# Optimization experiments

Hardware: AMD Instinct MI355X
Metric: run time of the kernel (lower is better)

The kernel has to match this reference:

```python
import jax, jax.numpy as jnp
import numpy as np
from jax import lax

B, S, D, E, H = 2, 2048, 1024, 8, 4096


def setup_inputs() -> dict:
    key = jax.random.key(0)
    ks = jax.random.split(key, 10)
    sc = 0.02  # GPT-style init scale
    return {
        "x": jax.random.normal(ks[0], (B, S, D), jnp.float32),
        "noise": jax.random.normal(ks[1], (B, S, E), jnp.float32),
        "w_route": jax.random.normal(ks[2], (D, E), jnp.float32) * sc,
        "b_route": jnp.zeros((E,), jnp.float32),
        "w_noise": jax.random.normal(ks[3], (D, E), jnp.float32) * sc,
        "b_noise": jnp.zeros((E,), jnp.float32),
        "w_fc": jax.random.normal(ks[4], (E, D, H), jnp.float32) * sc,
        "b_fc": jnp.zeros((E, H), jnp.float32),
        "w_proj": jax.random.normal(ks[5], (E, H, D), jnp.float32) * sc,
        "b_proj": jnp.zeros((E, D), jnp.float32),
        "top_k": 2,
    }


def reference(x, noise, w_route, b_route, w_noise, b_noise, w_fc, b_fc, w_proj, b_proj, top_k):
    # --- NoisyTopkRouter ---
    logits = x @ w_route + b_route                      # [B,S,E]
    noise_logits = x @ w_noise + b_noise                # [B,S,E]
    noisy = logits + noise * jax.nn.softplus(noise_logits)
    gate1 = jax.nn.softmax(noisy, axis=-1)              # dense gate (aux output)

    topk_vals, topk_idx = lax.top_k(noisy, top_k)       # [B,S,K]
    # softmax over sparse logits (-inf elsewhere) == softmax over the top-k values
    gk = jax.nn.softmax(topk_vals, axis=-1)             # [B,S,K]
    # scatter top-k gates back to the dense expert axis; non-selected experts get 0
    gating = (jax.nn.one_hot(topk_idx, E, dtype=x.dtype) * gk[..., None]).sum(-2)  # [B,S,E]

    # --- Experts (dense-over-experts, masked by gating; math identical to
    #     masked gather/scatter since non-selected gates are exactly 0) ---
    h = jnp.einsum('bsd,edh->bseh', x, w_fc) + b_fc     # [B,S,E,H]
    h = jax.nn.gelu(h, approximate=True)                # GELU(tanh)
    y = jnp.einsum('bseh,ehd->bsed', h, w_proj) + b_proj  # [B,S,E,D]
    out = jnp.einsum('bsed,bse->bsd', y, gating)        # weighted combine
    return out, gate1
```

## Files before the change

kernel.cpp:

```cpp
#include <hip/hip_runtime.h>
#include <cstdint>


#define DEV __device__ __forceinline__

typedef __attribute__((ext_vector_type(8))) short short8;
typedef __attribute__((ext_vector_type(4))) float floatx4;

constexpr int D_ = 1024, E_ = 8, H_ = 4096;
constexpr int NTOK = 4096;
constexpr int CAP  = 4096;
constexpr int TOTSLOT = NTOK * 2;

constexpr size_t O_COUNT = 0;
constexpr size_t O_OFFS  = 64;
constexpr size_t O_BTOK  = 128;
constexpr size_t O_BGATE = O_BTOK  + (size_t)E_ * CAP * 4;
constexpr size_t O_PAIR  = O_BGATE + (size_t)E_ * CAP * 4;
constexpr size_t O_XG    = (O_PAIR + (size_t)NTOK * 2 * 4 + 255) & ~(size_t)255;
constexpr size_t O_HBUF  = O_XG   + (size_t)TOTSLOT * D_ * 2;
constexpr size_t O_YBUF  = O_HBUF + (size_t)TOTSLOT * H_ * 2;
constexpr size_t O_WT    = O_YBUF + (size_t)TOTSLOT * D_ * 2;
constexpr size_t WS_NEED = O_WT   + (size_t)E_ * D_ * H_ * 2;

DEV float b2f(unsigned short u) {
    union { unsigned int i; float f; } v; v.i = ((unsigned int)u) << 16; return v.f;
}
DEV unsigned int f2b(float f) {
    union { float f; unsigned int i; } v; v.f = f;
    unsigned int r = v.i + 0x7fffu + ((v.i >> 16) & 1u);
    return (r >> 16) & 0xffffu;
}
DEV float gelu_tanh(float x) {
    float u = 0.7978845608028654f * (x + 0.044715f * x * x * x);
    u = fminf(fmaxf(u, -20.f), 20.f);
    float e = __expf(2.f * u);
    float t = (e - 1.f) / (e + 1.f);
    return 0.5f * x * (1.f + t);
}

typedef __attribute__((address_space(3))) unsigned int lds_u32_t;
typedef const __attribute__((address_space(1))) unsigned int g_u32_t;
DEV void gload16(const unsigned short* g, const unsigned short* l) {
    __builtin_amdgcn_global_load_lds((g_u32_t*)(size_t)g,
                                     (lds_u32_t*)(unsigned int)(size_t)l, 16, 0, 0);
}

__global__ __launch_bounds__(64) void zero_counts(int* counts) {
    if (threadIdx.x < E_) counts[threadIdx.x] = 0;
}

__global__ __launch_bounds__(256) void router_kernel(
    const float* __restrict__ x, const float* __restrict__ noise,
    const float* __restrict__ w_route, const float* __restrict__ b_route,
    const float* __restrict__ w_noise, const float* __restrict__ b_noise,
    float* __restrict__ out,
    int* counts, int* btok, float* bgate, int* pairs)
{
    int wave = threadIdx.x >> 6, lane = threadIdx.x & 63;
    int t = blockIdx.x * 4 + wave;

    double racc[E_], nacc[E_];
#pragma unroll
    for (int e = 0; e < E_; e++) { racc[e] = 0.0; nacc[e] = 0.0; }

#pragma unroll 4
    for (int i = 0; i < D_ / 64; i++) {
        int j = i * 64 + lane;
        float xv = x[(size_t)t * D_ + j];
        const float* wr = w_route + (size_t)j * E_;
        const float* wn = w_noise + (size_t)j * E_;
        float4 a0 = ((const float4*)wr)[0], a1 = ((const float4*)wr)[1];
        float4 c0 = ((const float4*)wn)[0], c1 = ((const float4*)wn)[1];
        const float rv[8] = {a0.x,a0.y,a0.z,a0.w,a1.x,a1.y,a1.z,a1.w};
        const float nv[8] = {c0.x,c0.y,c0.z,c0.w,c1.x,c1.y,c1.z,c1.w};
#pragma unroll
        for (int e = 0; e < E_; e++) {
            racc[e] += (double)(xv * rv[e]);
            nacc[e] += (double)(xv * nv[e]);
        }
    }
#pragma unroll
    for (int off = 32; off > 0; off >>= 1)
#pragma unroll
        for (int e = 0; e < E_; e++) {
            racc[e] += __shfl_down(racc[e], off);
            nacc[e] += __shfl_down(nacc[e], off);
        }

    if (lane == 0) {
        double nz[E_];
#pragma unroll
        for (int e = 0; e < E_; e++) {
            double lg = racc[e] + (double)b_route[e];
            double nl = nacc[e] + (double)b_noise[e];
            double sp = (nl > 0.0) ? nl + log1p(exp(-nl)) : log1p(exp(nl));
            nz[e] = lg + (double)noise[(size_t)t * E_ + e] * sp;
        }
        double mx = nz[0];
#pragma unroll
        for (int e = 1; e < E_; e++) mx = fmax(mx, nz[e]);
        double se = 0.0, ex[E_];
#pragma unroll
        for (int e = 0; e < E_; e++) { ex[e] = exp(nz[e] - mx); se += ex[e]; }
#pragma unroll
        for (int e = 0; e < E_; e++)
            out[(size_t)NTOK * D_ + (size_t)t * E_ + e] = (float)(ex[e] / se);
        double v0 = -1e300, v1 = -1e300; int i0 = 0, i1 = 0;
#pragma unroll
        for (int e = 0; e < E_; e++) {
            double v = nz[e];
            if (v > v0) { v1 = v0; i1 = i0; v0 = v; i0 = e; }
            else if (v > v1) { v1 = v; i1 = e; }
        }
        double g0 = 1.0 / (1.0 + exp(v1 - v0));
        float  g1 = (float)(1.0 - g0);
        int l0 = atomicAdd(&counts[i0], 1);
        int l1 = atomicAdd(&counts[i1], 1);
        btok[i0 * CAP + l0] = t;  bgate[i0 * CAP + l0] = (float)g0;
        btok[i1 * CAP + l1] = t;  bgate[i1 * CAP + l1] = g1;
        pairs[2 * t]     = (i0 << 16) | l0;
        pairs[2 * t + 1] = (i1 << 16) | l1;
    }
}

__global__ __launch_bounds__(64) void offsets_kernel(const int* counts, int* offs) {
    if (threadIdx.x == 0) {
        int a = 0;
        for (int e = 0; e < E_; e++) { offs[e] = a; a += counts[e]; }
        offs[E_] = a;
    }
}

__global__ __launch_bounds__(256) void gather_x(
    const float* __restrict__ x, const int* __restrict__ pairs,
    const int* __restrict__ offs, unsigned short* __restrict__ xg)
{
    int t = blockIdx.x;
    int c = threadIdx.x * 4;
    float4 v = *(const float4*)(x + (size_t)t * D_ + c);
    uint2 o;
    o.x = f2b(v.x) | (f2b(v.y) << 16);
    o.y = f2b(v.z) | (f2b(v.w) << 16);
    int p0 = pairs[2 * t], p1 = pairs[2 * t + 1];
    size_t r0 = (size_t)(offs[p0 >> 16] + (p0 & 0xffff)) * D_;
    size_t r1 = (size_t)(offs[p1 >> 16] + (p1 & 0xffff)) * D_;
    *(uint2*)(xg + r0 + c) = o;
    *(uint2*)(xg + r1 + c) = o;
}

__global__ __launch_bounds__(256) void transpose_w(
    const float* __restrict__ w, unsigned short* __restrict__ wT, int K, int N)
{
    __shared__ unsigned short t[64][65];
    const int e  = blockIdx.z;
    const int k0 = blockIdx.y * 64;
    const int n0 = blockIdx.x * 64;
    const int r  = threadIdx.x >> 2;
    const int c4 = (threadIdx.x & 3) * 16;
    const float* src = w + ((size_t)e * K + k0 + r) * N + n0 + c4;
#pragma unroll
    for (int i = 0; i < 4; i++) {
        float4 v = ((const float4*)src)[i];
        t[r][c4 + 4*i + 0] = (unsigned short)f2b(v.x);
        t[r][c4 + 4*i + 1] = (unsigned short)f2b(v.y);
        t[r][c4 + 4*i + 2] = (unsigned short)f2b(v.z);
        t[r][c4 + 4*i + 3] = (unsigned short)f2b(v.w);
    }
    __syncthreads();
    unsigned short* dstp = wT + ((size_t)e * N + n0 + r) * K + k0 + c4;
    unsigned short tmp[16];
#pragma unroll
    for (int i = 0; i < 16; i++) tmp[i] = t[c4 + i][r];
#pragma unroll
    for (int h = 0; h < 2; h++) {
        uint4 pk;
        pk.x = (unsigned int)tmp[8*h+0] | ((unsigned int)tmp[8*h+1] << 16);
        pk.y = (unsigned int)tmp[8*h+2] | ((unsigned int)tmp[8*h+3] << 16);
        pk.z = (unsigned int)tmp[8*h+4] | ((unsigned int)tmp[8*h+5] << 16);
        pk.w = (unsigned int)tmp[8*h+6] | ((unsigned int)tmp[8*h+7] << 16);
        ((uint4*)dstp)[h] = pk;
    }
}

__global__ __launch_bounds__(256) void zero_pbuf(float* pb0, float* pb1) {
    size_t i = ((size_t)blockIdx.x * 256 + threadIdx.x) * 4;
    float4 z = {0.f, 0.f, 0.f, 0.f};
    *(float4*)(pb0 + i) = z;
    *(float4*)(pb1 + i) = z;
}

template <int KD, int ND, bool FC, int KHALVES>
__global__ __launch_bounds__(256) void moe_gemm32(
    const unsigned short* __restrict__ A,
    const unsigned short* __restrict__ wT,
    const float* __restrict__ bias32,
    unsigned short* __restrict__ dstBf,
    float* __restrict__ pb0, float* __restrict__ pb1,
    const int* __restrict__ counts, const int* __restrict__ offs,
    const float* __restrict__ bgate)
{
    const int lin = blockIdx.x;
    const int xcd = lin & 7, slot = lin >> 3;
    int e, mt, nt, kh;
    if (FC) {
        nt = xcd * 4 + (slot & 3);
        mt = (slot >> 2) & 31;
        e  = slot >> 7;
        kh = 0;
    } else {
        nt = xcd;
        mt = slot & 31;
        kh = (slot >> 5) & 1;
        e  = slot >> 6;
    }
    const int cnt = counts[e];
    const int m0 = mt * 128;
    if (m0 >= cnt) return;
    const int n0 = nt * 128;
    const int off = offs[e];

    constexpr int KB = KD / KHALVES;
    const int kbase = kh * KB;

    __shared__ unsigned short smem[2][2 * 128 * 32];
    constexpr int BOFF = 128 * 32;

    const int tid = threadIdx.x;
    const int waveid = tid >> 6, lane = tid & 63;
    const int srow16 = lane >> 2;
    const int sslot  = lane & 3;

    const unsigned short* aAddr[2];
    const unsigned short* bAddr[2];
#pragma unroll
    for (int c = 0; c < 2; c++) {
        const int rl = (waveid * 2 + c) * 16 + srow16;
        const int g  = sslot ^ ((rl >> 1) & 3);
        int ar = m0 + rl;
        if (ar > cnt - 1) ar = cnt - 1;
        aAddr[c] = A + (size_t)(off + ar) * KD + kbase + g * 8;
        const int br = n0 + rl;
        bAddr[c] = wT + ((size_t)e * ND + br) * KD + kbase + g * 8;
    }

    const int wm = (waveid & 1) * 64, wn = (waveid >> 1) * 64;
    const int lrow = lane & 15, quad = lane >> 4;

    floatx4 acc[4][4];
#pragma unroll
    for (int fm = 0; fm < 4; fm++)
#pragma unroll
        for (int fn = 0; fn < 4; fn++) acc[fm][fn] = (floatx4)0.f;

    const int nk = KB / 32;

#pragma unroll
    for (int c = 0; c < 2; c++) {
        gload16(aAddr[c], &smem[0][(waveid * 2 + c) * 512]);
        gload16(bAddr[c], &smem[0][BOFF + (waveid * 2 + c) * 512]);
    }
    __syncthreads();

    for (int t = 0; t < nk; ++t) {
        const int cur = t & 1;
        if (t + 1 < nk) {
            const int k0 = (t + 1) * 32;
#pragma unroll
            for (int c = 0; c < 2; c++) {
                gload16(aAddr[c] + k0, &smem[cur ^ 1][(waveid * 2 + c) * 512]);
                gload16(bAddr[c] + k0, &smem[cur ^ 1][BOFF + (waveid * 2 + c) * 512]);
            }
        }
        const unsigned short* As = &smem[cur][0];
        const unsigned short* Bs = &smem[cur][BOFF];
        short8 af[4], bfr[4];
#pragma unroll
        for (int f = 0; f < 4; f++) {
            const int Ra = wm + f * 16 + lrow;
            const int Rb = wn + f * 16 + lrow;
            af[f]  = *(const short8*)&As[Ra * 32 + ((quad ^ ((Ra >> 1) & 3)) * 8)];
            bfr[f] = *(const short8*)&Bs[Rb * 32 + ((quad ^ ((Rb >> 1) & 3)) * 8)];
        }
#pragma unroll
        for (int fm = 0; fm < 4; fm++)
#pragma unroll
            for (int fn = 0; fn < 4; fn++)
                acc[fm][fn] = __builtin_amdgcn_mfma_f32_16x16x32_bf16(
                    af[fm], bfr[fn], acc[fm][fn], 0, 0, 0);
        __syncthreads();
    }

    const int gc = n0 + wn + lrow;
    float bcol[4];
#pragma unroll
    for (int fn = 0; fn < 4; fn++) bcol[fn] = bias32[(size_t)e * ND + gc + fn * 16];

#pragma unroll
    for (int fm = 0; fm < 4; fm++) {
        int srow0 = m0 + wm + fm * 16 + quad * 4;
#pragma unroll
        for (int r = 0; r < 4; r++) {
            int srow = srow0 + r;
            if (srow < cnt) {
                const int oslot = off + srow;
                if (FC) {
                    size_t base = (size_t)oslot * ND;
#pragma unroll
                    for (int fn = 0; fn < 4; fn++) {
                        float v = acc[fm][fn][r] + bcol[fn];
                        dstBf[base + gc + fn * 16] = (unsigned short)f2b(gelu_tanh(v));
                    }
                } else {
                    float gt = bgate[e * CAP + srow];
                    float* pb = (oslot < NTOK)
                        ? pb0 + (size_t)oslot * ND
                        : pb1 + (size_t)(oslot - NTOK) * ND;
#pragma unroll
                    for (int fn = 0; fn < 4; fn++) {
                        float v = (acc[fm][fn][r] + (kh == 0 ? bcol[fn] : 0.f)) * gt;
                        atomicAdd(&pb[gc + fn * 16], v);
                    }
                }
            }
        }
    }
}

__global__ __launch_bounds__(256) void combine_kernel(
    const float* __restrict__ pb0, const float* __restrict__ pb1,
    const int* __restrict__ pairs, const int* __restrict__ offs,
    float* __restrict__ out)
{
    int t = blockIdx.x;
    int p0 = pairs[2 * t], p1 = pairs[2 * t + 1];
    int s0 = offs[p0 >> 16] + (p0 & 0xffff);
    int s1 = offs[p1 >> 16] + (p1 & 0xffff);
    int c = threadIdx.x * 4;
    const float* a = (s0 < NTOK ? pb0 + (size_t)s0 * D_
                                : pb1 + (size_t)(s0 - NTOK) * D_) + c;
    const float* b = (s1 < NTOK ? pb0 + (size_t)s1 * D_
                                : pb1 + (size_t)(s1 - NTOK) * D_) + c;
    float4 va = *(const float4*)a;
    float4 vb = *(const float4*)b;
    float4 o;
    o.x = va.x + vb.x; o.y = va.y + vb.y; o.z = va.z + vb.z; o.w = va.w + vb.w;
    *(float4*)(out + (size_t)t * D_ + c) = o;
}

extern "C" void kernel_launch(void* const* d_in, const int* in_sizes, int n_in,
                              void* d_out, int out_size, void* d_ws, size_t ws_size,
                              hipStream_t stream) {
    if (ws_size < WS_NEED) return;

    const float* x       = (const float*)d_in[0];
    const float* noise   = (const float*)d_in[1];
    const float* w_route = (const float*)d_in[2];
    const float* b_route = (const float*)d_in[3];
    const float* w_noise = (const float*)d_in[4];
    const float* b_noise = (const float*)d_in[5];
    const float* w_fc    = (const float*)d_in[6];
    const float* b_fc    = (const float*)d_in[7];
    const float* w_proj  = (const float*)d_in[8];
    const float* b_proj  = (const float*)d_in[9];

    char* ws = (char*)d_ws;
    int*   counts = (int*)(ws + O_COUNT);
    int*   offs   = (int*)(ws + O_OFFS);
    int*   btok   = (int*)(ws + O_BTOK);
    float* bgate  = (float*)(ws + O_BGATE);
    int*   pairs  = (int*)(ws + O_PAIR);
    unsigned short* xg   = (unsigned short*)(ws + O_XG);
    unsigned short* hbuf = (unsigned short*)(ws + O_HBUF);
    unsigned short* wT   = (unsigned short*)(ws + O_WT);
    float* pb0 = (float*)(ws + O_XG);
    float* pb1 = (float*)(ws + O_YBUF);

    zero_counts<<<dim3(1), dim3(64), 0, stream>>>(counts);
    router_kernel<<<dim3(NTOK / 4), dim3(256), 0, stream>>>(
        x, noise, w_route, b_route, w_noise, b_noise, (float*)d_out,
        counts, btok, bgate, pairs);
    offsets_kernel<<<dim3(1), dim3(64), 0, stream>>>(counts, offs);
    gather_x<<<dim3(NTOK), dim3(256), 0, stream>>>(x, pairs, offs, xg);

    transpose_w<<<dim3(H_ / 64, D_ / 64, E_), dim3(256), 0, stream>>>(w_fc, wT, D_, H_);
    moe_gemm32<D_, H_, true, 1><<<dim3(8 * 32 * 32), dim3(256), 0, stream>>>(
        xg, wT, b_fc, hbuf, pb0, pb1, counts, offs, bgate);

    zero_pbuf<<<dim3(NTOK), dim3(256), 0, stream>>>(pb0, pb1);

    transpose_w<<<dim3(D_ / 64, H_ / 64, E_), dim3(256), 0, stream>>>(w_proj, wT, H_, D_);
    moe_gemm32<H_, D_, false, 2><<<dim3(8 * 32 * 2 * 8), dim3(256), 0, stream>>>(
        hbuf, wT, b_proj, nullptr, pb0, pb1, counts, offs, bgate);

    combine_kernel<<<dim3(NTOK), dim3(256), 0, stream>>>(pb0, pb1, pairs, offs, (float*)d_out);
}
```

Measured before the change: 704.0 us.

## Enlarge MoE GEMM tiles to 256x256 with 8 waves and 4-stage LDS pipeline

Replaces the 128x128, 4-wave expert GEMM with a 256x256 tile computed by 8 waves (512 threads), each wave holding an 8x4 MFMA accumulator grid. The double-buffered loop becomes a 4-stage prefetch pipeline in dynamic shared memory, with explicit vmcnt waits, barriers and setprio around the MFMA block. Block-index decoding is remapped for the new tile counts. The aim is higher arithmetic intensity and better latency hiding. In exchange it adds register pressure (launch bounds 512,2) and 128KB of LDS per block, and yields fewer, coarser blocks, which can hurt load balance for experts with small token counts.

```diff
diff --git a/kernel.cpp b/kernel.cpp
--- a/kernel.cpp
+++ b/kernel.cpp
@@ -191,7 +191,7 @@
 }
 
 template <int KD, int ND, bool FC, int KHALVES>
-__global__ __launch_bounds__(256) void moe_gemm32(
+__global__ __launch_bounds__(512, 2) void moe_gemm8w(
     const unsigned short* __restrict__ A,
     const unsigned short* __restrict__ wT,
     const float* __restrict__ bias32,
@@ -200,31 +200,33 @@
     const int* __restrict__ counts, const int* __restrict__ offs,
     const float* __restrict__ bgate)
 {
+    constexpr int BM = 256, BN = 256, BK = 32;
+    constexpr int SEG  = (BM + BN) * BK;
+    constexpr int BOFF = BM * BK;
+    extern __shared__ unsigned short smem[];
+
     const int lin = blockIdx.x;
     const int xcd = lin & 7, slot = lin >> 3;
     int e, mt, nt, kh;
     if (FC) {
-        nt = xcd * 4 + (slot & 3);
-        mt = (slot >> 2) & 31;
-        e  = slot >> 7;
+        nt = xcd * 2 + (slot & 1);
+        mt = (slot >> 1) & 15;
+        e  = slot >> 5;
         kh = 0;
     } else {
-        nt = xcd;
-        mt = slot & 31;
-        kh = (slot >> 5) & 1;
-        e  = slot >> 6;
+        nt = xcd & 3;
+        kh = xcd >> 2;
+        mt = slot & 15;
+        e  = slot >> 4;
     }
     const int cnt = counts[e];
-    const int m0 = mt * 128;
+    const int m0 = mt * BM;
     if (m0 >= cnt) return;
-    const int n0 = nt * 128;
+    const int n0 = nt * BN;
     const int off = offs[e];
-
     constexpr int KB = KD / KHALVES;
-    const int kbase = kh * KB;
-
-    __shared__ unsigned short smem[2][2 * 128 * 32];
-    constexpr int BOFF = 128 * 32;
+    constexpr int nk = KB / BK;
+    const int kbase = (KHALVES > 1) ? kh * KB : 0;
 
     const int tid = threadIdx.x;
     const int waveid = tid >> 6, lane = tid & 63;
@@ -244,52 +246,71 @@
         bAddr[c] = wT + ((size_t)e * ND + br) * KD + kbase + g * 8;
     }
 
-    const int wm = (waveid & 1) * 64, wn = (waveid >> 1) * 64;
+    const int wm = (waveid >> 2) * 128;
+    const int wn = (waveid & 3) * 64;
     const int lrow = lane & 15, quad = lane >> 4;
 
-    floatx4 acc[4][4];
-#pragma unroll
-    for (int fm = 0; fm < 4; fm++)
+    floatx4 acc[8][4];
+#pragma unroll
+    for (int fm = 0; fm < 8; fm++)
 #pragma unroll
         for (int fn = 0; fn < 4; fn++) acc[fm][fn] = (floatx4)0.f;
 
-    const int nk = KB / 32;
-
-#pragma unroll
-    for (int c = 0; c < 2; c++) {
-        gload16(aAddr[c], &smem[0][(waveid * 2 + c) * 512]);
-        gload16(bAddr[c], &smem[0][BOFF + (waveid * 2 + c) * 512]);
-    }
-    __syncthreads();
-
-    for (int t = 0; t < nk; ++t) {
-        const int cur = t & 1;
-        if (t + 1 < nk) {
-            const int k0 = (t + 1) * 32;
-#pragma unroll
-            for (int c = 0; c < 2; c++) {
-                gload16(aAddr[c] + k0, &smem[cur ^ 1][(waveid * 2 + c) * 512]);
-                gload16(bAddr[c] + k0, &smem[cur ^ 1][BOFF + (waveid * 2 + c) * 512]);
-            }
-        }
-        const unsigned short* As = &smem[cur][0];
-        const unsigned short* Bs = &smem[cur][BOFF];
-        short8 af[4], bfr[4];
-#pragma unroll
-        for (int f = 0; f < 4; f++) {
-            const int Ra = wm + f * 16 + lrow;
-            const int Rb = wn + f * 16 + lrow;
-            af[f]  = *(const short8*)&As[Ra * 32 + ((quad ^ ((Ra >> 1) & 3)) * 8)];
-            bfr[f] = *(const short8*)&Bs[Rb * 32 + ((quad ^ ((Rb >> 1) & 3)) * 8)];
-        }
-#pragma unroll
-        for (int fm = 0; fm < 4; fm++)
-#pragma unroll
-            for (int fn = 0; fn < 4; fn++)
-                acc[fm][fn] = __builtin_amdgcn_mfma_f32_16x16x32_bf16(
-                    af[fm], bfr[fn], acc[fm][fn], 0, 0, 0);
-        __syncthreads();
-    }
+#define STAGE(K_, S_) {                                                      \
+    unsigned short* bs_ = smem + (S_) * SEG;                                 \
+    const int ko_ = (K_) * BK;                                               \
+    _Pragma("unroll")                                                        \
+    for (int c = 0; c < 2; c++) {                                            \
+        gload16(aAddr[c] + ko_, &bs_[(waveid * 2 + c) * 512]);               \
+        gload16(bAddr[c] + ko_, &bs_[BOFF + (waveid * 2 + c) * 512]);        \
+    } }
+
+#define COMPUTE(S_) {                                                        \
+    const unsigned short* As_ = smem + (S_) * SEG;                           \
+    const unsigned short* Bs_ = As_ + BOFF;                                  \
+    short8 af_[8], bf_[4];                                                   \
+    _Pragma("unroll")                                                        \
+    for (int f = 0; f < 8; f++) {                                            \
+        const int R_ = wm + f * 16 + lrow;                                   \
+        af_[f] = *(const short8*)&As_[R_ * 32 + ((quad ^ ((R_ >> 1) & 3)) * 8)]; \
+    }                                                                        \
+    _Pragma("unroll")                                                        \
+    for (int f = 0; f < 4; f++) {                                            \
+        const int R_ = wn + f * 16 + lrow;                                   \
+        bf_[f] = *(const short8*)&Bs_[R_ * 32 + ((quad ^ ((R_ >> 1) & 3)) * 8)]; \
+    }                                                                        \
+    __builtin_amdgcn_s_setprio(1);                                           \
+    _Pragma("unroll")                                                        \
+    for (int fm = 0; fm < 8; fm++)                                           \
+        _Pragma("unroll")                                                    \
+        for (int fn = 0; fn < 4; fn++)                                       \
+            acc[fm][fn] = __builtin_amdgcn_mfma_f32_16x16x32_bf16(           \
+                af_[fm], bf_[fn], acc[fm][fn], 0, 0, 0);                     \
+    __builtin_amdgcn_s_setprio(0); }
+
+#define WAITBAR(VM_) {                                                       \
+    __builtin_amdgcn_sched_barrier(0);                                       \
+    asm volatile("s_waitcnt vmcnt(" #VM_ ") lgkmcnt(0)" ::: "memory");       \
+    __builtin_amdgcn_s_barrier();                                            \
+    __builtin_amdgcn_sched_barrier(0); }
+
+    STAGE(0, 0); STAGE(1, 1); STAGE(2, 2);
+    WAITBAR(8);
+
+    for (int t = 0; t < nk - 3; ++t) {
+        STAGE(t + 3, (t + 3) & 3);
+        COMPUTE(t & 3);
+        WAITBAR(8);
+    }
+    COMPUTE((nk - 3) & 3);
+    WAITBAR(4);
+    COMPUTE((nk - 2) & 3);
+    WAITBAR(0);
+    COMPUTE((nk - 1) & 3);
+
+#undef STAGE
+#undef COMPUTE
+#undef WAITBAR
 
     const int gc = n0 + wn + lrow;
     float bcol[4];
@@ -297,7 +318,7 @@
     for (int fn = 0; fn < 4; fn++) bcol[fn] = bias32[(size_t)e * ND + gc + fn * 16];
 
 #pragma unroll
-    for (int fm = 0; fm < 4; fm++) {
+    for (int fm = 0; fm < 8; fm++) {
         int srow0 = m0 + wm + fm * 16 + quad * 4;
 #pragma unroll
         for (int r = 0; r < 4; r++) {
@@ -314,8 +335,8 @@
                 } else {
                     float gt = bgate[e * CAP + srow];
                     float* pb = (oslot < NTOK)
-                        ? pb0 + (size_t)oslot * ND
-                        : pb1 + (size_t)(oslot - NTOK) * ND;
+                        ? pb0 + (size_t)oslot * D_
+                        : pb1 + (size_t)(oslot - NTOK) * D_;
 #pragma unroll
                     for (int fn = 0; fn < 4; fn++) {
                         float v = (acc[fm][fn][r] + (kh == 0 ? bcol[fn] : 0.f)) * gt;
@@ -376,6 +397,8 @@
     float* pb0 = (float*)(ws + O_XG);
     float* pb1 = (float*)(ws + O_YBUF);
 
+    constexpr unsigned GEMM_LDS = 4u * (256u + 256u) * 32u * 2u;
+
     zero_counts<<<dim3(1), dim3(64), 0, stream>>>(counts);
     router_kernel<<<dim3(NTOK / 4), dim3(256), 0, stream>>>(
         x, noise, w_route, b_route, w_noise, b_noise, (float*)d_out,
@@ -384,13 +407,13 @@
     gather_x<<<dim3(NTOK), dim3(256), 0, stream>>>(x, pairs, offs, xg);
 
     transpose_w<<<dim3(H_ / 64, D_ / 64, E_), dim3(256), 0, stream>>>(w_fc, wT, D_, H_);
-    moe_gemm32<D_, H_, true, 1><<<dim3(8 * 32 * 32), dim3(256), 0, stream>>>(
+    moe_gemm8w<D_, H_, true, 1><<<dim3(8 * 256), dim3(512), GEMM_LDS, stream>>>(
         xg, wT, b_fc, hbuf, pb0, pb1, counts, offs, bgate);
 
     zero_pbuf<<<dim3(NTOK), dim3(256), 0, stream>>>(pb0, pb1);
 
     transpose_w<<<dim3(D_ / 64, H_ / 64, E_), dim3(256), 0, stream>>>(w_proj, wT, H_, D_);
-    moe_gemm32<H_, D_, false, 2><<<dim3(8 * 32 * 2 * 8), dim3(256), 0, stream>>>(
+    moe_gemm8w<H_, D_, false, 2><<<dim3(8 * 128), dim3(512), GEMM_LDS, stream>>>(
         hbuf, wT, b_proj, nullptr, pb0, pb1, counts, offs, bgate);
 
     combine_kernel<<<dim3(NTOK), dim3(256), 0, stream>>>(pb0, pb1, pairs, offs, (float*)d_out);
```

After: 736.7 us. 4.6% more time.
